# Kernel optimization log

Measured on AMD Instinct MI355X. Metric: run time of the kernel, lower is better.

The kernel has to match this reference:

```python
import jax, jax.numpy as jnp
import numpy as np

N = 1024  # hidden_state
L = 16384  # sequence length


def setup_inputs() -> dict:
    key = jax.random.key(0)
    kA, kB, kC, kd, kX = jax.random.split(key, 5)
    # kaiming_normal_ with nonlinearity='linear': std = 1/sqrt(fan_in) = 1/sqrt(N)
    A = jax.random.normal(kA, (N, N), dtype=jnp.float32) / jnp.sqrt(jnp.float32(N))
    # nn.init.normal_(B, std=(1/N)**0.5)
    B = jax.random.normal(kB, (N, 1), dtype=jnp.float32) / jnp.sqrt(jnp.float32(N))
    # nn.init.normal_(C, std=1.0)
    C = jax.random.normal(kC, (1, N), dtype=jnp.float32)
    D = jnp.ones((1,), dtype=jnp.float32)
    # uniform in [log(min_delta), log(max_delta)]
    log_delta = jax.random.uniform(kd, (1,), dtype=jnp.float32,
                                   minval=jnp.log(1e-3), maxval=jnp.log(1e-1))
    X = jax.random.normal(kX, (L,), dtype=jnp.float32)
    return {"X": X, "A": A, "B": B, "C": C, "D": D, "log_delta": log_delta}


def _discretize(A, B, log_delta):
    n = A.shape[0]
    I = jnp.eye(n, dtype=A.dtype)
    d = jnp.exp(log_delta)  # (1,) broadcasts
    A1 = I - d * 0.5 * A
    A2 = I + d * 0.5 * A
    A1_inv = jnp.linalg.inv(A1)
    dA = A1_inv @ A2                 # (N, N) bilinear (Tustin) discretization
    dB = (A1_inv @ (d * B))[:, 0]    # (N,)
    return dA, dB


def reference(X, A, B, C, D, log_delta):
    """S4 RNN-mode forward: linear state-space recurrence + skip connection."""
    dA, dB = _discretize(A, B, log_delta)
    c = C[0]  # (N,)

    def step(h, x):
        # h_k = dA @ h_{k-1} + dB * x_k ; y_k = C @ h_k
        h = dA @ h + dB * x
        return h, c @ h

    h0 = jnp.zeros((A.shape[0],), dtype=A.dtype)  # cache_h_k starts at zeros
    _, ys = jax.lax.scan(step, h0, X)             # ys: (L,)
    return ys + D * X                              # skip = D * X
```

## Files before the change

kernel.cpp:

```cpp
#include <hip/hip_runtime.h>
#include <math.h>

#define N1 1024
#define NN2 (N1*N1)
#define LL 16384

__global__ __launch_bounds__(256) void k_scale(const float* __restrict__ A,
                                               const float* __restrict__ logd,
                                               float* __restrict__ e) {
    int i = blockIdx.x * 256 + threadIdx.x;
    float d = expf(logd[0]);
    e[i] = 0.5f * d * A[i];
}

__global__ __launch_bounds__(256) void k_add(const float* __restrict__ a,
                                             const float* __restrict__ b,
                                             float* __restrict__ o) {
    int i = blockIdx.x * 256 + threadIdx.x;
    o[i] = a[i] + b[i];
}

__device__ __forceinline__ void chain_part(const float* __restrict__ M,
                                           float* __restrict__ V,
                                           float* __restrict__ CP,
                                           int w, int lkc, int mode, int cb,
                                           float* sV, float (*red)[64]) {
    int kc = 1 << lkc;
    int i = cb >> (4 + lkc);
    int ky = (cb >> 4) & (kc - 1);
    int nx = cb & 15;
    int mlen = N1 >> lkc;
    int m0 = ky * mlen, n0 = nx * 64;
    int t = threadIdx.x;
    const float* Vi = V + (size_t)i * N1 + m0;
    if (t * 4 < mlen) *(float4*)&sV[t * 4] = *(const float4*)&Vi[t * 4];
    __syncthreads();
    int wave = t >> 6, lane = t & 63;
    if (mode == 0) {
        for (int rr = 0; rr < 16; ++rr) {
            int n = n0 + wave * 16 + rr;
            const float* Mr = M + (size_t)n * N1 + m0;
            float acc = 0.f;
            for (int m = lane * 4; m < mlen; m += 256) {
                float4 a = *(const float4*)&Mr[m];
                float4 v = *(const float4*)&sV[m];
                acc += a.x * v.x + a.y * v.y + a.z * v.z + a.w * v.w;
            }
#pragma unroll
            for (int off = 32; off > 0; off >>= 1) acc += __shfl_down(acc, off, 64);
            if (lane == 0) {
                if (kc == 1) V[(size_t)(w + i) * N1 + n] = sV[n] + acc;
                else CP[((size_t)i * kc + ky) * N1 + n] = acc;
            }
        }
    } else {
        int n = n0 + lane;
        int msub = mlen >> 2;
        int mb = wave * msub;
        float acc = 0.f;
#pragma unroll 8
        for (int m = 0; m < msub; ++m)
            acc += sV[mb + m] * M[(size_t)(m0 + mb + m) * N1 + n];
        red[wave][lane] = acc;
        __syncthreads();
        if (t < 64) {
            float s = red[0][t] + red[1][t] + red[2][t] + red[3][t];
            if (kc == 1) V[(size_t)(w + i) * N1 + n0 + t] = sV[n0 + t] + s;
            else CP[((size_t)i * kc + ky) * N1 + n0 + t] = s;
        }
    }
}

__global__ __launch_bounds__(256) void k_fused(const float* __restrict__ Ain,
                                               const float* __restrict__ Bin,
                                               float* __restrict__ part,
                                               float* __restrict__ V,
                                               float* __restrict__ CP,
                                               int w, int lkc, int nchain, int mode) {
    __shared__ float As[2][32][68];
    __shared__ float Bs[2][32][68];
    __shared__ float sV[N1];
    __shared__ float red[4][64];
    int b = blockIdx.x;
    if (b < nchain) {
        chain_part(Ain, V, CP, w, lkc, mode, b, sV, red);
        return;
    }
    int g = b - nchain;
    int t = threadIdx.x;
    int z = g >> 8, ty = (g >> 4) & 15, tx = g & 15;
    int m0 = ty * 64, n0 = tx * 64, kz = z * 512;
    int tm = (t & 15) * 4, tn = (t >> 4) * 4;
    int lmA = t >> 2, lkA = (t & 3) * 8;
    int kbB = t >> 3, nbB = (t & 7) * 8;
    const float* Ap = Ain + (size_t)(m0 + lmA) * N1 + kz + lkA;
    const float* Bp = Bin + (size_t)(kz + kbB) * N1 + n0 + nbB;

    float4 pa0 = *(const float4*)(Ap);
    float4 pa1 = *(const float4*)(Ap + 4);
    float4 pb0 = *(const float4*)(Bp);
    float4 pb1 = *(const float4*)(Bp + 4);
    As[0][lkA + 0][lmA] = pa0.x; As[0][lkA + 1][lmA] = pa0.y;
    As[0][lkA + 2][lmA] = pa0.z; As[0][lkA + 3][lmA] = pa0.w;
    As[0][lkA + 4][lmA] = pa1.x; As[0][lkA + 5][lmA] = pa1.y;
    As[0][lkA + 6][lmA] = pa1.z; As[0][lkA + 7][lmA] = pa1.w;
    *(float4*)&Bs[0][kbB][nbB]     = pb0;
    *(float4*)&Bs[0][kbB][nbB + 4] = pb1;
    __syncthreads();

    float acc[4][4];
#pragma unroll
    for (int i = 0; i < 4; ++i)
#pragma unroll
        for (int j = 0; j < 4; ++j) acc[i][j] = 0.f;

    for (int tt = 0; tt < 16; ++tt) {
        int cur = tt & 1;
        float4 na0, na1, nb0, nb1;
        if (tt < 15) {
            int k0 = (tt + 1) * 32;
            na0 = *(const float4*)(Ap + k0);
            na1 = *(const float4*)(Ap + k0 + 4);
            nb0 = *(const float4*)(Bp + (size_t)k0 * N1);
            nb1 = *(const float4*)(Bp + (size_t)k0 * N1 + 4);
        }
#pragma unroll
        for (int k = 0; k < 32; ++k) {
            float4 a = *(float4*)&As[cur][k][tm];
            float4 bb = *(float4*)&Bs[cur][k][tn];
            acc[0][0] += a.x * bb.x; acc[0][1] += a.x * bb.y; acc[0][2] += a.x * bb.z; acc[0][3] += a.x * bb.w;
            acc[1][0] += a.y * bb.x; acc[1][1] += a.y * bb.y; acc[1][2] += a.y * bb.z; acc[1][3] += a.y * bb.w;
            acc[2][0] += a.z * bb.x; acc[2][1] += a.z * bb.y; acc[2][2] += a.z * bb.z; acc[2][3] += a.z * bb.w;
            acc[3][0] += a.w * bb.x; acc[3][1] += a.w * bb.y; acc[3][2] += a.w * bb.z; acc[3][3] += a.w * bb.w;
        }
        if (tt < 15) {
            int nxt = cur ^ 1;
            As[nxt][lkA + 0][lmA] = na0.x; As[nxt][lkA + 1][lmA] = na0.y;
            As[nxt][lkA + 2][lmA] = na0.z; As[nxt][lkA + 3][lmA] = na0.w;
            As[nxt][lkA + 4][lmA] = na1.x; As[nxt][lkA + 5][lmA] = na1.y;
            As[nxt][lkA + 6][lmA] = na1.z; As[nxt][lkA + 7][lmA] = na1.w;
            *(float4*)&Bs[nxt][kbB][nbB]     = nb0;
            *(float4*)&Bs[nxt][kbB][nbB + 4] = nb1;
            __syncthreads();
        }
    }
    float* Po = part + (size_t)z * NN2;
#pragma unroll
    for (int i = 0; i < 4; ++i) {
        float4 o = {acc[i][0], acc[i][1], acc[i][2], acc[i][3]};
        *(float4*)&Po[(size_t)(m0 + tm + i) * N1 + n0 + tn] = o;
    }
}

__global__ __launch_bounds__(256) void k_cpart(const float* __restrict__ M,
                                               float* __restrict__ V,
                                               float* __restrict__ CP,
                                               int w, int lkc, int mode) {
    __shared__ float sV[N1];
    __shared__ float red[4][64];
    chain_part(M, V, CP, w, lkc, mode, blockIdx.x, sV, red);
}

__global__ __launch_bounds__(256) void k_redu(const float* __restrict__ part,
                                              const float* __restrict__ Aadd,
                                              float* __restrict__ C,
                                              float alpha, float beta,
                                              float* __restrict__ V,
                                              const float* __restrict__ CP,
                                              int w, int kc) {
    int b = blockIdx.x, t = threadIdx.x;
    if (b < 1024) {
        int i = (b * 256 + t) * 4;
        float4 p0 = *(const float4*)&part[i];
        float4 p1 = *(const float4*)&part[NN2 + i];
        float4 av = *(const float4*)&Aadd[i];
        float4 o;
        o.x = alpha * (p0.x + p1.x) + beta * av.x;
        o.y = alpha * (p0.y + p1.y) + beta * av.y;
        o.z = alpha * (p0.z + p1.z) + beta * av.z;
        o.w = alpha * (p0.w + p1.w) + beta * av.w;
        *(float4*)&C[i] = o;
    } else {
        int rb = b - 1024;
        int i = rb >> 2;
        int n = (rb & 3) * 256 + t;
        const float* pp = CP + (size_t)i * kc * N1 + n;
        float s = 0.f;
        for (int c = 0; c < kc; ++c) s += pp[(size_t)c * N1];
        V[(size_t)(w + i) * N1 + n] = V[(size_t)i * N1 + n] + s;
    }
}

__global__ __launch_bounds__(256) void k_initR(const float* __restrict__ Bv,
                                               const float* __restrict__ Cv,
                                               const float* __restrict__ logd,
                                               const float* __restrict__ part,
                                               float* __restrict__ Q,
                                               float* __restrict__ P) {
    int n = blockIdx.x * 256 + threadIdx.x;
    float s = 0.f;
    for (int c = 0; c < 16; ++c) s += part[(size_t)c * N1 + n];
    float d = expf(logd[0]);
    Q[n] = d * (Bv[n] + 0.5f * s);
    P[n] = Cv[n];
}

__global__ __launch_bounds__(256) void k_kdot(const float* __restrict__ P,
                                              const float* __restrict__ Q,
                                              float* __restrict__ K) {
    int t = threadIdx.x;
    int wid = blockIdx.x * 4 + (t >> 6), lane = t & 63;
    int a = wid >> 7, b = wid & 127;
    const float* Pr = P + (size_t)a * N1;
    const float* Qr = Q + (size_t)b * N1;
    float acc = 0.f;
#pragma unroll
    for (int jj = 0; jj < 4; ++jj) {
        int m = jj * 256 + lane * 4;
        float4 p = *(const float4*)&Pr[m];
        float4 q = *(const float4*)&Qr[m];
        acc += p.x * q.x + p.y * q.y + p.z * q.z + p.w * q.w;
    }
#pragma unroll
    for (int off = 32; off > 0; off >>= 1) acc += __shfl_down(acc, off, 64);
    if (lane == 0) K[wid] = acc;
}

__global__ __launch_bounds__(256) void k_conv1(const float* __restrict__ X,
                                               const float* __restrict__ K,
                                               float* __restrict__ part) {
    __shared__ __align__(16) float ks[1280];
    __shared__ __align__(16) float xs[256];
    int bx = blockIdx.x, tt = threadIdx.x;
    int o = 0;
    while (bx >= 2 * (o + 1) * (o + 1) + 2 * (o + 1)) ++o;
    int jt = bx - (2 * o * o + 2 * o);
    int T0 = o * 1024, J0 = jt * 256;
    int mb = T0 - J0 - 255;
    for (int ii = tt; ii < 1280; ii += 256) {
        int m = mb + ii;
        ks[ii] = (m >= 0 && m < LL) ? K[m] : 0.f;
    }
    xs[tt] = X[J0 + tt];
    __syncthreads();

    float acc0 = 0.f, acc1 = 0.f, acc2 = 0.f, acc3 = 0.f;
    int base0 = 4 * tt + 252;
#pragma unroll 4
    for (int jj = 0; jj < 256; jj += 4) {
        float4 xv  = *(const float4*)&xs[jj];
        float4 kv0 = *(const float4*)&ks[base0 - jj];
        float4 kv1 = *(const float4*)&ks[base0 - jj + 4];
        float kk0 = kv0.x, kk1 = kv0.y, kk2 = kv0.z, kk3 = kv0.w;
        float kk4 = kv1.x, kk5 = kv1.y, kk6 = kv1.z;
        acc0 += kk3 * xv.x + kk2 * xv.y + kk1 * xv.z + kk0 * xv.w;
        acc1 += kk4 * xv.x + kk3 * xv.y + kk2 * xv.z + kk1 * xv.w;
        acc2 += kk5 * xv.x + kk4 * xv.y + kk3 * xv.z + kk2 * xv.w;
        acc3 += kk6 * xv.x + kk5 * xv.y + kk4 * xv.z + kk3 * xv.w;
    }
    float4 out = {acc0, acc1, acc2, acc3};
    *(float4*)&part[((size_t)(o * 64 + jt)) * 1024 + 4 * tt] = out;
}

__global__ __launch_bounds__(256) void k_conv2(const float* __restrict__ X,
                                               const float* __restrict__ part,
                                               const float* __restrict__ Dp,
                                               float* __restrict__ Y) {
    int o = blockIdx.x, tt = threadIdx.x;
    int c = 4 * tt;
    float s0 = 0.f, s1 = 0.f, s2 = 0.f, s3 = 0.f;
    int cnt = 4 * o + 4;
    for (int jt = 0; jt < cnt; ++jt) {
        float4 p = *(const float4*)&part[((size_t)(o * 64 + jt)) * 1024 + c];
        s0 += p.x; s1 += p.y; s2 += p.z; s3 += p.w;
    }
    float dsk = Dp[0];
    int t = o * 1024 + c;
    float4 xv = *(const float4*)&X[t];
    float4 out;
    out.x = dsk * xv.x + s0;
    out.y = dsk * xv.y + s1;
    out.z = dsk * xv.z + s2;
    out.w = dsk * xv.w + s3;
    *(float4*)&Y[t] = out;
}

extern "C" void kernel_launch(void* const* d_in, const int* in_sizes, int n_in,
                              void* d_out, int out_size, void* d_ws, size_t ws_size,
                              hipStream_t stream) {
    const float* X    = (const float*)d_in[0];
    const float* A    = (const float*)d_in[1];
    const float* Bv   = (const float*)d_in[2];
    const float* Cv   = (const float*)d_in[3];
    const float* Dp   = (const float*)d_in[4];
    const float* logd = (const float*)d_in[5];
    float* ws = (float*)d_ws;

    float* S0 = ws;
    float* S1 = ws + (size_t)NN2;
    float* S2 = ws + 2*(size_t)NN2;
    float* S3 = ws + 3*(size_t)NN2;
    float* S4 = ws + 4*(size_t)NN2;
    float* MP = ws + 5*(size_t)NN2;
    float* CP = ws + 7*(size_t)NN2;
    float* Q  = CP + 64*(size_t)N1;
    float* P  = Q + 128*(size_t)N1;
    float* Kc = P + 128*(size_t)N1;
    float* Y  = (float*)d_out;

    k_scale<<<4096, 256, 0, stream>>>(A, logd, S0);
    k_fused<<<512, 256, 0, stream>>>(S0, S0, MP, nullptr, nullptr, 0, 0, 0, 0);
    k_redu<<<1024, 256, 0, stream>>>(MP, S0, S1, 1.f, 0.f, nullptr, nullptr, 0, 0);
    k_fused<<<512, 256, 0, stream>>>(S1, S1, MP, nullptr, nullptr, 0, 0, 0, 0);
    k_redu<<<1024, 256, 0, stream>>>(MP, S1, S2, 1.f, 1.f, nullptr, nullptr, 0, 0);
    k_add<<<4096, 256, 0, stream>>>(S0, S1, S3);
    k_fused<<<512, 256, 0, stream>>>(S3, S2, MP, nullptr, nullptr, 0, 0, 0, 0);
    k_redu<<<1024, 256, 0, stream>>>(MP, S3, S4, 2.f, 2.f, nullptr, nullptr, 0, 0);

    k_cpart<<<256, 256, 0, stream>>>(S4, (float*)Bv, CP, 1, 4, 0);
    k_initR<<<4, 256, 0, stream>>>(Bv, Cv, logd, CP, Q, P);

    float* cur = S4;
    float* nxt = S0;
    for (int k = 0; k < 7; ++k) {
        int w = 1 << k;
        int lkc = (w < 16) ? (4 - k) : 0;
        int kc = 1 << lkc;
        int nchain = 16 * kc * w;
        int nR = (kc > 1) ? 4 * w : 0;
        k_fused<<<nchain + 512, 256, 0, stream>>>(cur, cur, MP, Q, CP, w, lkc, nchain, 0);
        k_redu<<<1024 + nR, 256, 0, stream>>>(MP, cur, nxt, 1.f, 2.f, Q, CP, w, kc);
        float* tsw = cur; cur = nxt; nxt = tsw;
    }
    for (int k = 0; k < 6; ++k) {
        int w = 1 << k;
        int lkc = (w < 16) ? (4 - k) : 0;
        int kc = 1 << lkc;
        int nchain = 16 * kc * w;
        int nR = (kc > 1) ? 4 * w : 0;
        k_fused<<<nchain + 512, 256, 0, stream>>>(cur, cur, MP, P, CP, w, lkc, nchain, 1);
        k_redu<<<1024 + nR, 256, 0, stream>>>(MP, cur, nxt, 1.f, 2.f, P, CP, w, kc);
        float* tsw = cur; cur = nxt; nxt = tsw;
    }
    k_cpart<<<1024, 256, 0, stream>>>(cur, P, CP, 64, 0, 1);

    k_kdot<<<4096, 256, 0, stream>>>(P, Q, Kc);
    k_conv1<<<544, 256, 0, stream>>>(X, Kc, MP);
    k_conv2<<<16, 256, 0, stream>>>(X, MP, Dp, Y);
}
```

Before: 795.7 us.

## Replace FP32 SIMT matrix squaring with split-bf16 MFMA GEMMs

Each 1024x1024 matrix product is now computed on bf16 MFMA units. Operands are split into three bf16 pieces and six cross-term MFMAs are issued, approximating FP32 accuracy. The reduction kernel also emits the row-major split and a transposed split of its output, so the next squaring reads pre-packed operands. This removes the FP32 FMA-bound inner loop, at the cost of extra split and transpose writes, more bytes per operand, and a possible precision loss from dropping the small cross terms.

```diff
diff --git a/kernel.cpp b/kernel.cpp
--- a/kernel.cpp
+++ b/kernel.cpp
@@ -4,20 +4,23 @@
 #define N1 1024
 #define NN2 (N1*N1)
 #define LL 16384
-
-__global__ __launch_bounds__(256) void k_scale(const float* __restrict__ A,
-                                               const float* __restrict__ logd,
-                                               float* __restrict__ e) {
-    int i = blockIdx.x * 256 + threadIdx.x;
-    float d = expf(logd[0]);
-    e[i] = 0.5f * d * A[i];
-}
-
-__global__ __launch_bounds__(256) void k_add(const float* __restrict__ a,
-                                             const float* __restrict__ b,
-                                             float* __restrict__ o) {
-    int i = blockIdx.x * 256 + threadIdx.x;
-    o[i] = a[i] + b[i];
+#define PSTR 40
+
+typedef unsigned short u16;
+typedef __attribute__((ext_vector_type(8))) short bffrag;
+typedef __attribute__((ext_vector_type(4))) float f32x4;
+
+__device__ __forceinline__ u16 bf16rne(float x, float& rem) {
+    unsigned u = __float_as_uint(x);
+    u16 h = (u16)((u + 0x7FFF + ((u >> 16) & 1)) >> 16);
+    rem = x - __uint_as_float((unsigned)h << 16);
+    return h;
+}
+__device__ __forceinline__ void split3(float x, u16& h0, u16& h1, u16& h2) {
+    float r1, r2, r3;
+    h0 = bf16rne(x, r1);
+    h1 = bf16rne(r1, r2);
+    h2 = bf16rne(r2, r3);
 }
 
 __device__ __forceinline__ void chain_part(const float* __restrict__ M,
@@ -71,85 +74,98 @@
     }
 }
 
-__global__ __launch_bounds__(256) void k_fused(const float* __restrict__ Ain,
-                                               const float* __restrict__ Bin,
-                                               float* __restrict__ part,
-                                               float* __restrict__ V,
-                                               float* __restrict__ CP,
-                                               int w, int lkc, int nchain, int mode) {
-    __shared__ float As[2][32][68];
-    __shared__ float Bs[2][32][68];
+__global__ __launch_bounds__(256, 1) void k_mfma(const u16* __restrict__ RA,
+                                                 const u16* __restrict__ TB,
+                                                 float* __restrict__ part,
+                                                 const float* __restrict__ Dm,
+                                                 float* __restrict__ V,
+                                                 float* __restrict__ CP,
+                                                 int w, int lkc, int nchain, int mode) {
+    __shared__ u16 Asl[3][64][PSTR];
+    __shared__ u16 Bsl[3][64][PSTR];
     __shared__ float sV[N1];
     __shared__ float red[4][64];
     int b = blockIdx.x;
     if (b < nchain) {
-        chain_part(Ain, V, CP, w, lkc, mode, b, sV, red);
+        chain_part(Dm, V, CP, w, lkc, mode, b, sV, red);
         return;
     }
     int g = b - nchain;
     int t = threadIdx.x;
-    int z = g >> 8, ty = (g >> 4) & 15, tx = g & 15;
+    int z = g >> 8;
+    int ty = (g >> 4) & 15, tx = g & 15;
     int m0 = ty * 64, n0 = tx * 64, kz = z * 512;
-    int tm = (t & 15) * 4, tn = (t >> 4) * 4;
-    int lmA = t >> 2, lkA = (t & 3) * 8;
-    int kbB = t >> 3, nbB = (t & 7) * 8;
-    const float* Ap = Ain + (size_t)(m0 + lmA) * N1 + kz + lkA;
-    const float* Bp = Bin + (size_t)(kz + kbB) * N1 + n0 + nbB;
-
-    float4 pa0 = *(const float4*)(Ap);
-    float4 pa1 = *(const float4*)(Ap + 4);
-    float4 pb0 = *(const float4*)(Bp);
-    float4 pb1 = *(const float4*)(Bp + 4);
-    As[0][lkA + 0][lmA] = pa0.x; As[0][lkA + 1][lmA] = pa0.y;
-    As[0][lkA + 2][lmA] = pa0.z; As[0][lkA + 3][lmA] = pa0.w;
-    As[0][lkA + 4][lmA] = pa1.x; As[0][lkA + 5][lmA] = pa1.y;
-    As[0][lkA + 6][lmA] = pa1.z; As[0][lkA + 7][lmA] = pa1.w;
-    *(float4*)&Bs[0][kbB][nbB]     = pb0;
-    *(float4*)&Bs[0][kbB][nbB + 4] = pb1;
-    __syncthreads();
-
-    float acc[4][4];
-#pragma unroll
-    for (int i = 0; i < 4; ++i)
-#pragma unroll
-        for (int j = 0; j < 4; ++j) acc[i][j] = 0.f;
-
-    for (int tt = 0; tt < 16; ++tt) {
-        int cur = tt & 1;
-        float4 na0, na1, nb0, nb1;
-        if (tt < 15) {
-            int k0 = (tt + 1) * 32;
-            na0 = *(const float4*)(Ap + k0);
-            na1 = *(const float4*)(Ap + k0 + 4);
-            nb0 = *(const float4*)(Bp + (size_t)k0 * N1);
-            nb1 = *(const float4*)(Bp + (size_t)k0 * N1 + 4);
+    int srow = t >> 2, sk = (t & 3) * 8;
+    int wave = t >> 6, lane = t & 63;
+    int mq = (wave & 1) * 32, nq = (wave >> 1) * 32;
+    int fl = lane & 15, kg8 = (lane >> 4) * 8;
+
+    const size_t abase = (size_t)(m0 + srow) * N1 + kz + sk;
+    const size_t bbase = (size_t)(n0 + srow) * N1 + kz + sk;
+
+    uint4 pa[3], pb[3];
+#pragma unroll
+    for (int p = 0; p < 3; ++p) {
+        pa[p] = *(const uint4*)&RA[(size_t)p * NN2 + abase];
+        pb[p] = *(const uint4*)&TB[(size_t)p * NN2 + bbase];
+    }
+
+    f32x4 acc[2][2];
+#pragma unroll
+    for (int mi = 0; mi < 2; ++mi)
+#pragma unroll
+        for (int nj = 0; nj < 2; ++nj) acc[mi][nj] = (f32x4){0.f, 0.f, 0.f, 0.f};
+
+    for (int kt = 0; kt < 16; ++kt) {
+#pragma unroll
+        for (int p = 0; p < 3; ++p) {
+            *(uint4*)&Asl[p][srow][sk] = pa[p];
+            *(uint4*)&Bsl[p][srow][sk] = pb[p];
         }
-#pragma unroll
-        for (int k = 0; k < 32; ++k) {
-            float4 a = *(float4*)&As[cur][k][tm];
-            float4 bb = *(float4*)&Bs[cur][k][tn];
-            acc[0][0] += a.x * bb.x; acc[0][1] += a.x * bb.y; acc[0][2] += a.x * bb.z; acc[0][3] += a.x * bb.w;
-            acc[1][0] += a.y * bb.x; acc[1][1] += a.y * bb.y; acc[1][2] += a.y * bb.z; acc[1][3] += a.y * bb.w;
-            acc[2][0] += a.z * bb.x; acc[2][1] += a.z * bb.y; acc[2][2] += a.z * bb.z; acc[2][3] += a.z * bb.w;
-            acc[3][0] += a.w * bb.x; acc[3][1] += a.w * bb.y; acc[3][2] += a.w * bb.z; acc[3][3] += a.w * bb.w;
+        __syncthreads();
+        if (kt < 15) {
+            size_t koff = (size_t)(kt + 1) * 32;
+#pragma unroll
+            for (int p = 0; p < 3; ++p) {
+                pa[p] = *(const uint4*)&RA[(size_t)p * NN2 + abase + koff];
+                pb[p] = *(const uint4*)&TB[(size_t)p * NN2 + bbase + koff];
+            }
         }
-        if (tt < 15) {
-            int nxt = cur ^ 1;
-            As[nxt][lkA + 0][lmA] = na0.x; As[nxt][lkA + 1][lmA] = na0.y;
-            As[nxt][lkA + 2][lmA] = na0.z; As[nxt][lkA + 3][lmA] = na0.w;
-            As[nxt][lkA + 4][lmA] = na1.x; As[nxt][lkA + 5][lmA] = na1.y;
-            As[nxt][lkA + 6][lmA] = na1.z; As[nxt][lkA + 7][lmA] = na1.w;
-            *(float4*)&Bs[nxt][kbB][nbB]     = nb0;
-            *(float4*)&Bs[nxt][kbB][nbB + 4] = nb1;
-            __syncthreads();
+        bffrag a[2][3], bb[2][3];
+#pragma unroll
+        for (int mi = 0; mi < 2; ++mi)
+#pragma unroll
+            for (int p = 0; p < 3; ++p)
+                a[mi][p] = *(bffrag*)&Asl[p][mq + mi * 16 + fl][kg8];
+#pragma unroll
+        for (int nj = 0; nj < 2; ++nj)
+#pragma unroll
+            for (int q = 0; q < 3; ++q)
+                bb[nj][q] = *(bffrag*)&Bsl[q][nq + nj * 16 + fl][kg8];
+#pragma unroll
+        for (int mi = 0; mi < 2; ++mi)
+#pragma unroll
+            for (int nj = 0; nj < 2; ++nj) {
+                acc[mi][nj] = __builtin_amdgcn_mfma_f32_16x16x32_bf16(a[mi][0], bb[nj][0], acc[mi][nj], 0, 0, 0);
+                acc[mi][nj] = __builtin_amdgcn_mfma_f32_16x16x32_bf16(a[mi][0], bb[nj][1], acc[mi][nj], 0, 0, 0);
+                acc[mi][nj] = __builtin_amdgcn_mfma_f32_16x16x32_bf16(a[mi][1], bb[nj][0], acc[mi][nj], 0, 0, 0);
+                acc[mi][nj] = __builtin_amdgcn_mfma_f32_16x16x32_bf16(a[mi][0], bb[nj][2], acc[mi][nj], 0, 0, 0);
+                acc[mi][nj] = __builtin_amdgcn_mfma_f32_16x16x32_bf16(a[mi][1], bb[nj][1], acc[mi][nj], 0, 0, 0);
+                acc[mi][nj] = __builtin_amdgcn_mfma_f32_16x16x32_bf16(a[mi][2], bb[nj][0], acc[mi][nj], 0, 0, 0);
+            }
+        __syncthreads();
+    }
+    float* Po = part + (size_t)z * NN2;
+#pragma unroll
+    for (int mi = 0; mi < 2; ++mi)
+#pragma unroll
+        for (int nj = 0; nj < 2; ++nj) {
+            int row0 = m0 + mq + mi * 16 + (lane >> 4) * 4;
+            int col = n0 + nq + nj * 16 + fl;
+#pragma unroll
+            for (int r = 0; r < 4; ++r)
+                Po[(size_t)(row0 + r) * N1 + col] = acc[mi][nj][r];
         }
-    }
-    float* Po = part + (size_t)z * NN2;
-#pragma unroll
-    for (int i = 0; i < 4; ++i) {
-        float4 o = {acc[i][0], acc[i][1], acc[i][2], acc[i][3]};
-        *(float4*)&Po[(size_t)(m0 + tm + i) * N1 + n0 + tn] = o;
-    }
 }
 
 __global__ __launch_bounds__(256) void k_cpart(const float* __restrict__ M,
@@ -161,25 +177,103 @@
     chain_part(M, V, CP, w, lkc, mode, blockIdx.x, sV, red);
 }
 
-__global__ __launch_bounds__(256) void k_redu(const float* __restrict__ part,
-                                              const float* __restrict__ Aadd,
-                                              float* __restrict__ C,
-                                              float alpha, float beta,
-                                              float* __restrict__ V,
-                                              const float* __restrict__ CP,
-                                              int w, int kc) {
+__global__ __launch_bounds__(256) void k_split(const float* __restrict__ in1,
+                                               const float* __restrict__ in2,
+                                               const float* __restrict__ logd,
+                                               float c1,
+                                               float* __restrict__ outX,
+                                               u16* __restrict__ Rp,
+                                               u16* __restrict__ Tp) {
+    __shared__ float tile[32][33];
+    int b = blockIdx.x, t = threadIdx.x;
+    int bx = b & 31, by = b >> 5;
+    int x0 = bx * 32, y0 = by * 32;
+    int r = t >> 3, c4 = (t & 7) * 4;
+    float a = c1 * (logd ? expf(logd[0]) : 1.f);
+    size_t idx = (size_t)(y0 + r) * N1 + x0 + c4;
+    float4 v1 = *(const float4*)&in1[idx];
+    float4 X;
+    X.x = a * v1.x; X.y = a * v1.y; X.z = a * v1.z; X.w = a * v1.w;
+    if (in2) {
+        float4 v2 = *(const float4*)&in2[idx];
+        X.x += v2.x; X.y += v2.y; X.z += v2.z; X.w += v2.w;
+    }
+    *(float4*)&outX[idx] = X;
+    ushort4 h0, h1, h2;
+    split3(X.x, h0.x, h1.x, h2.x);
+    split3(X.y, h0.y, h1.y, h2.y);
+    split3(X.z, h0.z, h1.z, h2.z);
+    split3(X.w, h0.w, h1.w, h2.w);
+    *(ushort4*)&Rp[idx] = h0;
+    *(ushort4*)&Rp[(size_t)NN2 + idx] = h1;
+    *(ushort4*)&Rp[2 * (size_t)NN2 + idx] = h2;
+    tile[r][c4 + 0] = X.x; tile[r][c4 + 1] = X.y;
+    tile[r][c4 + 2] = X.z; tile[r][c4 + 3] = X.w;
+    __syncthreads();
+    if (Tp) {
+        int n = t >> 3, mb = (t & 7) * 4;
+        ushort4 g0, g1, g2;
+        float xv0 = tile[mb + 0][n], xv1 = tile[mb + 1][n];
+        float xv2 = tile[mb + 2][n], xv3 = tile[mb + 3][n];
+        split3(xv0, g0.x, g1.x, g2.x);
+        split3(xv1, g0.y, g1.y, g2.y);
+        split3(xv2, g0.z, g1.z, g2.z);
+        split3(xv3, g0.w, g1.w, g2.w);
+        size_t tidx = (size_t)(x0 + n) * N1 + y0 + mb;
+        *(ushort4*)&Tp[tidx] = g0;
+        *(ushort4*)&Tp[(size_t)NN2 + tidx] = g1;
+        *(ushort4*)&Tp[2 * (size_t)NN2 + tidx] = g2;
+    }
+}
+
+__global__ __launch_bounds__(256) void k_redusplit(const float* __restrict__ part,
+                                                   const float* __restrict__ Aadd,
+                                                   float* __restrict__ C,
+                                                   float alpha, float beta,
+                                                   u16* __restrict__ Rp,
+                                                   u16* __restrict__ Tp,
+                                                   float* __restrict__ V,
+                                                   const float* __restrict__ CP,
+                                                   int w, int kc) {
+    __shared__ float tile[32][33];
     int b = blockIdx.x, t = threadIdx.x;
     if (b < 1024) {
-        int i = (b * 256 + t) * 4;
-        float4 p0 = *(const float4*)&part[i];
-        float4 p1 = *(const float4*)&part[NN2 + i];
-        float4 av = *(const float4*)&Aadd[i];
-        float4 o;
-        o.x = alpha * (p0.x + p1.x) + beta * av.x;
-        o.y = alpha * (p0.y + p1.y) + beta * av.y;
-        o.z = alpha * (p0.z + p1.z) + beta * av.z;
-        o.w = alpha * (p0.w + p1.w) + beta * av.w;
-        *(float4*)&C[i] = o;
+        int bx = b & 31, by = b >> 5;
+        int x0 = bx * 32, y0 = by * 32;
+        int r = t >> 3, c4 = (t & 7) * 4;
+        size_t idx = (size_t)(y0 + r) * N1 + x0 + c4;
+        float4 p0 = *(const float4*)&part[idx];
+        float4 p1 = *(const float4*)&part[(size_t)NN2 + idx];
+        float4 av = *(const float4*)&Aadd[idx];
+        float4 X;
+        X.x = alpha * (p0.x + p1.x) + beta * av.x;
+        X.y = alpha * (p0.y + p1.y) + beta * av.y;
+        X.z = alpha * (p0.z + p1.z) + beta * av.z;
+        X.w = alpha * (p0.w + p1.w) + beta * av.w;
+        *(float4*)&C[idx] = X;
+        ushort4 h0, h1, h2;
+        split3(X.x, h0.x, h1.x, h2.x);
+        split3(X.y, h0.y, h1.y, h2.y);
+        split3(X.z, h0.z, h1.z, h2.z);
+        split3(X.w, h0.w, h1.w, h2.w);
+        *(ushort4*)&Rp[idx] = h0;
+        *(ushort4*)&Rp[(size_t)NN2 + idx] = h1;
+        *(ushort4*)&Rp[2 * (size_t)NN2 + idx] = h2;
+        tile[r][c4 + 0] = X.x; tile[r][c4 + 1] = X.y;
+        tile[r][c4 + 2] = X.z; tile[r][c4 + 3] = X.w;
+        __syncthreads();
+        int n = t >> 3, mb = (t & 7) * 4;
+        ushort4 g0, g1, g2;
+        float xv0 = tile[mb + 0][n], xv1 = tile[mb + 1][n];
+        float xv2 = tile[mb + 2][n], xv3 = tile[mb + 3][n];
+        split3(xv0, g0.x, g1.x, g2.x);
+        split3(xv1, g0.y, g1.y, g2.y);
+        split3(xv2, g0.z, g1.z, g2.z);
+        split3(xv3, g0.w, g1.w, g2.w);
+        size_t tidx = (size_t)(x0 + n) * N1 + y0 + mb;
+        *(ushort4*)&Tp[tidx] = g0;
+        *(ushort4*)&Tp[(size_t)NN2 + tidx] = g1;
+        *(ushort4*)&Tp[2 * (size_t)NN2 + tidx] = g2;
     } else {
         int rb = b - 1024;
         int i = rb >> 2;
@@ -302,23 +396,26 @@
     float* S3 = ws + 3*(size_t)NN2;
     float* S4 = ws + 4*(size_t)NN2;
     float* MP = ws + 5*(size_t)NN2;
-    float* CP = ws + 7*(size_t)NN2;
-    float* Q  = CP + 64*(size_t)N1;
-    float* P  = Q + 128*(size_t)N1;
-    float* Kc = P + 128*(size_t)N1;
+    float* CPb = ws + 7*(size_t)NN2;
+    float* Qv = CPb + 64*(size_t)N1;
+    float* Pv = Qv + 128*(size_t)N1;
+    float* Kc = Pv + 128*(size_t)N1;
+    u16*   R0 = (u16*)(Kc + LL);
+    u16*   R1 = R0 + 3*(size_t)NN2;
+    u16*   T0 = R1 + 3*(size_t)NN2;
     float* Y  = (float*)d_out;
 
-    k_scale<<<4096, 256, 0, stream>>>(A, logd, S0);
-    k_fused<<<512, 256, 0, stream>>>(S0, S0, MP, nullptr, nullptr, 0, 0, 0, 0);
-    k_redu<<<1024, 256, 0, stream>>>(MP, S0, S1, 1.f, 0.f, nullptr, nullptr, 0, 0);
-    k_fused<<<512, 256, 0, stream>>>(S1, S1, MP, nullptr, nullptr, 0, 0, 0, 0);
-    k_redu<<<1024, 256, 0, stream>>>(MP, S1, S2, 1.f, 1.f, nullptr, nullptr, 0, 0);
-    k_add<<<4096, 256, 0, stream>>>(S0, S1, S3);
-    k_fused<<<512, 256, 0, stream>>>(S3, S2, MP, nullptr, nullptr, 0, 0, 0, 0);
-    k_redu<<<1024, 256, 0, stream>>>(MP, S3, S4, 2.f, 2.f, nullptr, nullptr, 0, 0);
-
-    k_cpart<<<256, 256, 0, stream>>>(S4, (float*)Bv, CP, 1, 4, 0);
-    k_initR<<<4, 256, 0, stream>>>(Bv, Cv, logd, CP, Q, P);
+    k_split<<<1024, 256, 0, stream>>>(A, nullptr, logd, 0.5f, S0, R0, T0);
+    k_mfma<<<512, 256, 0, stream>>>(R0, T0, MP, nullptr, nullptr, nullptr, 0, 0, 0, 0);
+    k_redusplit<<<1024, 256, 0, stream>>>(MP, S0, S1, 1.f, 0.f, R0, T0, nullptr, nullptr, 0, 1);
+    k_mfma<<<512, 256, 0, stream>>>(R0, T0, MP, nullptr, nullptr, nullptr, 0, 0, 0, 0);
+    k_redusplit<<<1024, 256, 0, stream>>>(MP, S1, S2, 1.f, 1.f, R0, T0, nullptr, nullptr, 0, 1);
+    k_split<<<1024, 256, 0, stream>>>(S1, S0, nullptr, 1.f, S3, R1, nullptr);
+    k_mfma<<<512, 256, 0, stream>>>(R1, T0, MP, nullptr, nullptr, nullptr, 0, 0, 0, 0);
+    k_redusplit<<<1024, 256, 0, stream>>>(MP, S3, S4, 2.f, 2.f, R0, T0, nullptr, nullptr, 0, 1);
+
+    k_cpart<<<256, 256, 0, stream>>>(S4, (float*)Bv, CPb, 1, 4, 0);
+    k_initR<<<4, 256, 0, stream>>>(Bv, Cv, logd, CPb, Qv, Pv);
 
     float* cur = S4;
     float* nxt = S0;
@@ -328,8 +425,8 @@
         int kc = 1 << lkc;
         int nchain = 16 * kc * w;
         int nR = (kc > 1) ? 4 * w : 0;
-        k_fused<<<nchain + 512, 256, 0, stream>>>(cur, cur, MP, Q, CP, w, lkc, nchain, 0);
-        k_redu<<<1024 + nR, 256, 0, stream>>>(MP, cur, nxt, 1.f, 2.f, Q, CP, w, kc);
+        k_mfma<<<nchain + 512, 256, 0, stream>>>(R0, T0, MP, cur, Qv, CPb, w, lkc, nchain, 0);
+        k_redusplit<<<1024 + nR, 256, 0, stream>>>(MP, cur, nxt, 1.f, 2.f, R0, T0, Qv, CPb, w, kc);
         float* tsw = cur; cur = nxt; nxt = tsw;
     }
     for (int k = 0; k < 6; ++k) {
@@ -338,13 +435,13 @@
         int kc = 1 << lkc;
         int nchain = 16 * kc * w;
         int nR = (kc > 1) ? 4 * w : 0;
-        k_fused<<<nchain + 512, 256, 0, stream>>>(cur, cur, MP, P, CP, w, lkc, nchain, 1);
-        k_redu<<<1024 + nR, 256, 0, stream>>>(MP, cur, nxt, 1.f, 2.f, P, CP, w, kc);
+        k_mfma<<<nchain + 512, 256, 0, stream>>>(R0, T0, MP, cur, Pv, CPb, w, lkc, nchain, 1);
+        k_redusplit<<<1024 + nR, 256, 0, stream>>>(MP, cur, nxt, 1.f, 2.f, R0, T0, Pv, CPb, w, kc);
         float* tsw = cur; cur = nxt; nxt = tsw;
     }
-    k_cpart<<<1024, 256, 0, stream>>>(cur, P, CP, 64, 0, 1);
-
-    k_kdot<<<4096, 256, 0, stream>>>(P, Q, Kc);
+    k_cpart<<<1024, 256, 0, stream>>>(cur, Pv, CPb, 64, 0, 1);
+
+    k_kdot<<<4096, 256, 0, stream>>>(Pv, Qv, Kc);
     k_conv1<<<544, 256, 0, stream>>>(X, Kc, MP);
     k_conv2<<<16, 256, 0, stream>>>(X, MP, Dp, Y);
 }
```

Measured after the change: 1.280 ms. 60.9% more time.

## Fuse split-K reduction into GEMM via atomic tile flags and trim power chain

Applied to the files above, without the earlier changes.

Each split-K GEMM block now increments a per-tile atomic counter after writing its partial. The second block to finish sums both partials and applies the alpha/beta epilogue in place, which removes the separate reduction kernel after every squaring step. The chain-vector updates are simplified to a single full-length pass per block, and the transposed-chain squaring stops after four steps. The last three doublings are replaced by repeated matrix-vector applications with the final power. The change relies on threadfence/atomic ordering across blocks and on resetting the flags correctly, and it adds more small kernel launches at the tail.

```diff
diff --git a/kernel.cpp b/kernel.cpp
--- a/kernel.cpp
+++ b/kernel.cpp
@@ -5,12 +5,18 @@
 #define NN2 (N1*N1)
 #define LL 16384
 
-__global__ __launch_bounds__(256) void k_scale(const float* __restrict__ A,
-                                               const float* __restrict__ logd,
-                                               float* __restrict__ e) {
-    int i = blockIdx.x * 256 + threadIdx.x;
-    float d = expf(logd[0]);
-    e[i] = 0.5f * d * A[i];
+__global__ __launch_bounds__(256) void k_prep(const float* __restrict__ A,
+                                              const float* __restrict__ logd,
+                                              float* __restrict__ e,
+                                              int* __restrict__ flags) {
+    int b = blockIdx.x, t = threadIdx.x;
+    if (b < 4096) {
+        int i = b * 256 + t;
+        float d = expf(logd[0]);
+        e[i] = 0.5f * d * A[i];
+    } else {
+        if (t < 256) flags[t] = 0;
+    }
 }
 
 __global__ __launch_bounds__(256) void k_add(const float* __restrict__ a,
@@ -20,92 +26,85 @@
     o[i] = a[i] + b[i];
 }
 
-__device__ __forceinline__ void chain_part(const float* __restrict__ M,
-                                           float* __restrict__ V,
-                                           float* __restrict__ CP,
-                                           int w, int lkc, int mode, int cb,
-                                           float* sV, float (*red)[64]) {
-    int kc = 1 << lkc;
-    int i = cb >> (4 + lkc);
-    int ky = (cb >> 4) & (kc - 1);
-    int nx = cb & 15;
-    int mlen = N1 >> lkc;
-    int m0 = ky * mlen, n0 = nx * 64;
-    int t = threadIdx.x;
-    const float* Vi = V + (size_t)i * N1 + m0;
-    if (t * 4 < mlen) *(float4*)&sV[t * 4] = *(const float4*)&Vi[t * 4];
-    __syncthreads();
-    int wave = t >> 6, lane = t & 63;
-    if (mode == 0) {
-        for (int rr = 0; rr < 16; ++rr) {
-            int n = n0 + wave * 16 + rr;
-            const float* Mr = M + (size_t)n * N1 + m0;
+__global__ __launch_bounds__(256) void k_fused(const float* __restrict__ GA,
+                                               const float* __restrict__ GB,
+                                               float* __restrict__ MP,
+                                               float* __restrict__ Cout,
+                                               const float* __restrict__ Aadd,
+                                               float alpha, float beta,
+                                               int* __restrict__ flags,
+                                               const float* __restrict__ Dm,
+                                               float* __restrict__ V,
+                                               int w, int mode) {
+    __shared__ __align__(16) char smem[34816];
+    __shared__ int sflag;
+    int b = blockIdx.x, t = threadIdx.x;
+
+    if (b >= 512) {
+        int cb = b - 512;
+        int i = cb >> 4, nx = cb & 15, n0 = nx * 64;
+        float* sV  = (float*)smem;
+        float* red = (float*)(smem + 4096);
+        const float* Vi = V + (size_t)i * N1;
+        *(float4*)&sV[t * 4] = *(const float4*)&Vi[t * 4];
+        __syncthreads();
+        int wave = t >> 6, lane = t & 63;
+        if (mode == 0) {
+            for (int rr = 0; rr < 16; ++rr) {
+                int n = n0 + wave * 16 + rr;
+                const float* Mr = Dm + (size_t)n * N1;
+                float acc = 0.f;
+#pragma unroll
+                for (int jj = 0; jj < 4; ++jj) {
+                    int m = jj * 256 + lane * 4;
+                    float4 a = *(const float4*)&Mr[m];
+                    float4 v = *(const float4*)&sV[m];
+                    acc += a.x * v.x + a.y * v.y + a.z * v.z + a.w * v.w;
+                }
+#pragma unroll
+                for (int off = 32; off > 0; off >>= 1) acc += __shfl_down(acc, off, 64);
+                if (lane == 0) V[(size_t)(w + i) * N1 + n] = sV[n] + acc;
+            }
+        } else {
+            int n = n0 + lane;
+            int mb = wave * 256;
             float acc = 0.f;
-            for (int m = lane * 4; m < mlen; m += 256) {
-                float4 a = *(const float4*)&Mr[m];
-                float4 v = *(const float4*)&sV[m];
-                acc += a.x * v.x + a.y * v.y + a.z * v.z + a.w * v.w;
+#pragma unroll 8
+            for (int m = 0; m < 256; ++m)
+                acc += sV[mb + m] * Dm[(size_t)(mb + m) * N1 + n];
+            red[wave * 64 + lane] = acc;
+            __syncthreads();
+            if (t < 64) {
+                float s = red[t] + red[64 + t] + red[128 + t] + red[192 + t];
+                V[(size_t)(w + i) * N1 + n0 + t] = sV[n0 + t] + s;
             }
-#pragma unroll
-            for (int off = 32; off > 0; off >>= 1) acc += __shfl_down(acc, off, 64);
-            if (lane == 0) {
-                if (kc == 1) V[(size_t)(w + i) * N1 + n] = sV[n] + acc;
-                else CP[((size_t)i * kc + ky) * N1 + n] = acc;
-            }
-        }
-    } else {
-        int n = n0 + lane;
-        int msub = mlen >> 2;
-        int mb = wave * msub;
-        float acc = 0.f;
-#pragma unroll 8
-        for (int m = 0; m < msub; ++m)
-            acc += sV[mb + m] * M[(size_t)(m0 + mb + m) * N1 + n];
-        red[wave][lane] = acc;
-        __syncthreads();
-        if (t < 64) {
-            float s = red[0][t] + red[1][t] + red[2][t] + red[3][t];
-            if (kc == 1) V[(size_t)(w + i) * N1 + n0 + t] = sV[n0 + t] + s;
-            else CP[((size_t)i * kc + ky) * N1 + n0 + t] = s;
-        }
-    }
-}
-
-__global__ __launch_bounds__(256) void k_fused(const float* __restrict__ Ain,
-                                               const float* __restrict__ Bin,
-                                               float* __restrict__ part,
-                                               float* __restrict__ V,
-                                               float* __restrict__ CP,
-                                               int w, int lkc, int nchain, int mode) {
-    __shared__ float As[2][32][68];
-    __shared__ float Bs[2][32][68];
-    __shared__ float sV[N1];
-    __shared__ float red[4][64];
-    int b = blockIdx.x;
-    if (b < nchain) {
-        chain_part(Ain, V, CP, w, lkc, mode, b, sV, red);
+        }
         return;
     }
-    int g = b - nchain;
-    int t = threadIdx.x;
+
+    float* As = (float*)smem;
+    float* Bs = (float*)(smem + 17408);
+#define AS(bf, k, m) As[((bf) * 32 + (k)) * 68 + (m)]
+#define BS(bf, k, m) Bs[((bf) * 32 + (k)) * 68 + (m)]
+    int g = b;
     int z = g >> 8, ty = (g >> 4) & 15, tx = g & 15;
     int m0 = ty * 64, n0 = tx * 64, kz = z * 512;
     int tm = (t & 15) * 4, tn = (t >> 4) * 4;
     int lmA = t >> 2, lkA = (t & 3) * 8;
     int kbB = t >> 3, nbB = (t & 7) * 8;
-    const float* Ap = Ain + (size_t)(m0 + lmA) * N1 + kz + lkA;
-    const float* Bp = Bin + (size_t)(kz + kbB) * N1 + n0 + nbB;
+    const float* Ap = GA + (size_t)(m0 + lmA) * N1 + kz + lkA;
+    const float* Bp = GB + (size_t)(kz + kbB) * N1 + n0 + nbB;
 
     float4 pa0 = *(const float4*)(Ap);
     float4 pa1 = *(const float4*)(Ap + 4);
     float4 pb0 = *(const float4*)(Bp);
     float4 pb1 = *(const float4*)(Bp + 4);
-    As[0][lkA + 0][lmA] = pa0.x; As[0][lkA + 1][lmA] = pa0.y;
-    As[0][lkA + 2][lmA] = pa0.z; As[0][lkA + 3][lmA] = pa0.w;
-    As[0][lkA + 4][lmA] = pa1.x; As[0][lkA + 5][lmA] = pa1.y;
-    As[0][lkA + 6][lmA] = pa1.z; As[0][lkA + 7][lmA] = pa1.w;
-    *(float4*)&Bs[0][kbB][nbB]     = pb0;
-    *(float4*)&Bs[0][kbB][nbB + 4] = pb1;
+    AS(0, lkA + 0, lmA) = pa0.x; AS(0, lkA + 1, lmA) = pa0.y;
+    AS(0, lkA + 2, lmA) = pa0.z; AS(0, lkA + 3, lmA) = pa0.w;
+    AS(0, lkA + 4, lmA) = pa1.x; AS(0, lkA + 5, lmA) = pa1.y;
+    AS(0, lkA + 6, lmA) = pa1.z; AS(0, lkA + 7, lmA) = pa1.w;
+    *(float4*)&BS(0, kbB, nbB)     = pb0;
+    *(float4*)&BS(0, kbB, nbB + 4) = pb1;
     __syncthreads();
 
     float acc[4][4];
@@ -126,80 +125,117 @@
         }
 #pragma unroll
         for (int k = 0; k < 32; ++k) {
-            float4 a = *(float4*)&As[cur][k][tm];
-            float4 bb = *(float4*)&Bs[cur][k][tn];
+            float4 a = *(float4*)&AS(cur, k, tm);
+            float4 bb = *(float4*)&BS(cur, k, tn);
             acc[0][0] += a.x * bb.x; acc[0][1] += a.x * bb.y; acc[0][2] += a.x * bb.z; acc[0][3] += a.x * bb.w;
             acc[1][0] += a.y * bb.x; acc[1][1] += a.y * bb.y; acc[1][2] += a.y * bb.z; acc[1][3] += a.y * bb.w;
             acc[2][0] += a.z * bb.x; acc[2][1] += a.z * bb.y; acc[2][2] += a.z * bb.z; acc[2][3] += a.z * bb.w;
             acc[3][0] += a.w * bb.x; acc[3][1] += a.w * bb.y; acc[3][2] += a.w * bb.z; acc[3][3] += a.w * bb.w;
         }
         if (tt < 15) {
-            int nxt = cur ^ 1;
-            As[nxt][lkA + 0][lmA] = na0.x; As[nxt][lkA + 1][lmA] = na0.y;
-            As[nxt][lkA + 2][lmA] = na0.z; As[nxt][lkA + 3][lmA] = na0.w;
-            As[nxt][lkA + 4][lmA] = na1.x; As[nxt][lkA + 5][lmA] = na1.y;
-            As[nxt][lkA + 6][lmA] = na1.z; As[nxt][lkA + 7][lmA] = na1.w;
-            *(float4*)&Bs[nxt][kbB][nbB]     = nb0;
-            *(float4*)&Bs[nxt][kbB][nbB + 4] = nb1;
+            int nx_ = cur ^ 1;
+            AS(nx_, lkA + 0, lmA) = na0.x; AS(nx_, lkA + 1, lmA) = na0.y;
+            AS(nx_, lkA + 2, lmA) = na0.z; AS(nx_, lkA + 3, lmA) = na0.w;
+            AS(nx_, lkA + 4, lmA) = na1.x; AS(nx_, lkA + 5, lmA) = na1.y;
+            AS(nx_, lkA + 6, lmA) = na1.z; AS(nx_, lkA + 7, lmA) = na1.w;
+            *(float4*)&BS(nx_, kbB, nbB)     = nb0;
+            *(float4*)&BS(nx_, kbB, nbB + 4) = nb1;
             __syncthreads();
         }
     }
-    float* Po = part + (size_t)z * NN2;
+    float* Po = MP + (size_t)z * NN2;
 #pragma unroll
     for (int i = 0; i < 4; ++i) {
         float4 o = {acc[i][0], acc[i][1], acc[i][2], acc[i][3]};
         *(float4*)&Po[(size_t)(m0 + tm + i) * N1 + n0 + tn] = o;
     }
-}
-
-__global__ __launch_bounds__(256) void k_cpart(const float* __restrict__ M,
-                                               float* __restrict__ V,
-                                               float* __restrict__ CP,
-                                               int w, int lkc, int mode) {
+    __threadfence();
+    if (t == 0) sflag = atomicAdd(&flags[ty * 16 + tx], 1);
+    __syncthreads();
+    if (sflag == 1) {
+        __threadfence();
+        const float* Pq = MP + (size_t)(1 - z) * NN2;
+#pragma unroll
+        for (int i = 0; i < 4; ++i) {
+            size_t ri = (size_t)(m0 + tm + i) * N1 + n0 + tn;
+            float4 oth = *(const float4*)&Pq[ri];
+            float4 mine = {acc[i][0], acc[i][1], acc[i][2], acc[i][3]};
+            float4 p0 = (z == 0) ? mine : oth;
+            float4 p1 = (z == 0) ? oth : mine;
+            float4 av = *(const float4*)&Aadd[ri];
+            float4 o;
+            o.x = alpha * (p0.x + p1.x) + beta * av.x;
+            o.y = alpha * (p0.y + p1.y) + beta * av.y;
+            o.z = alpha * (p0.z + p1.z) + beta * av.z;
+            o.w = alpha * (p0.w + p1.w) + beta * av.w;
+            *(float4*)&Cout[ri] = o;
+        }
+        if (t == 0) flags[ty * 16 + tx] = 0;
+    }
+#undef AS
+#undef BS
+}
+
+__global__ __launch_bounds__(256) void k_capply(const float* __restrict__ M,
+                                                const float* __restrict__ src,
+                                                float* __restrict__ dst) {
     __shared__ float sV[N1];
     __shared__ float red[4][64];
-    chain_part(M, V, CP, w, lkc, mode, blockIdx.x, sV, red);
-}
-
-__global__ __launch_bounds__(256) void k_redu(const float* __restrict__ part,
-                                              const float* __restrict__ Aadd,
-                                              float* __restrict__ C,
-                                              float alpha, float beta,
-                                              float* __restrict__ V,
-                                              const float* __restrict__ CP,
-                                              int w, int kc) {
     int b = blockIdx.x, t = threadIdx.x;
-    if (b < 1024) {
-        int i = (b * 256 + t) * 4;
-        float4 p0 = *(const float4*)&part[i];
-        float4 p1 = *(const float4*)&part[NN2 + i];
-        float4 av = *(const float4*)&Aadd[i];
-        float4 o;
-        o.x = alpha * (p0.x + p1.x) + beta * av.x;
-        o.y = alpha * (p0.y + p1.y) + beta * av.y;
-        o.z = alpha * (p0.z + p1.z) + beta * av.z;
-        o.w = alpha * (p0.w + p1.w) + beta * av.w;
-        *(float4*)&C[i] = o;
-    } else {
-        int rb = b - 1024;
-        int i = rb >> 2;
-        int n = (rb & 3) * 256 + t;
-        const float* pp = CP + (size_t)i * kc * N1 + n;
-        float s = 0.f;
-        for (int c = 0; c < kc; ++c) s += pp[(size_t)c * N1];
-        V[(size_t)(w + i) * N1 + n] = V[(size_t)i * N1 + n] + s;
+    int i = b >> 4, nx = b & 15, n0 = nx * 64;
+    const float* Si = src + (size_t)i * N1;
+    *(float4*)&sV[t * 4] = *(const float4*)&Si[t * 4];
+    __syncthreads();
+    int wave = t >> 6, lane = t & 63;
+    int n = n0 + lane;
+    int mb = wave * 256;
+    float acc = 0.f;
+#pragma unroll 8
+    for (int m = 0; m < 256; ++m)
+        acc += sV[mb + m] * M[(size_t)(mb + m) * N1 + n];
+    red[wave][lane] = acc;
+    __syncthreads();
+    if (t < 64) {
+        float s = red[0][t] + red[1][t] + red[2][t] + red[3][t];
+        dst[(size_t)i * N1 + n0 + t] = sV[n0 + t] + s;
+    }
+}
+
+__global__ __launch_bounds__(256) void k_cpart(const float* __restrict__ M,
+                                               const float* __restrict__ Bv,
+                                               float* __restrict__ CP) {
+    __shared__ float sV[64];
+    int cb = blockIdx.x, t = threadIdx.x;
+    int ky = (cb >> 4) & 15, nx = cb & 15;
+    int m0 = ky * 64, n0 = nx * 64;
+    if (t < 16) *(float4*)&sV[t * 4] = *(const float4*)&Bv[m0 + t * 4];
+    __syncthreads();
+    int wave = t >> 6, lane = t & 63;
+    for (int rr = 0; rr < 16; ++rr) {
+        int n = n0 + wave * 16 + rr;
+        const float* Mr = M + (size_t)n * N1 + m0;
+        float acc = 0.f;
+        if (lane < 16) {
+            int m = lane * 4;
+            float4 a = *(const float4*)&Mr[m];
+            float4 v = *(const float4*)&sV[m];
+            acc = a.x * v.x + a.y * v.y + a.z * v.z + a.w * v.w;
+        }
+#pragma unroll
+        for (int off = 8; off > 0; off >>= 1) acc += __shfl_down(acc, off, 64);
+        if (lane == 0) CP[(size_t)ky * N1 + n] = acc;
     }
 }
 
 __global__ __launch_bounds__(256) void k_initR(const float* __restrict__ Bv,
                                                const float* __restrict__ Cv,
                                                const float* __restrict__ logd,
-                                               const float* __restrict__ part,
+                                               const float* __restrict__ CP,
                                                float* __restrict__ Q,
                                                float* __restrict__ P) {
     int n = blockIdx.x * 256 + threadIdx.x;
     float s = 0.f;
-    for (int c = 0; c < 16; ++c) s += part[(size_t)c * N1 + n];
+    for (int c = 0; c < 16; ++c) s += CP[(size_t)c * N1 + n];
     float d = expf(logd[0]);
     Q[n] = d * (Bv[n] + 0.5f * s);
     P[n] = Cv[n];
@@ -298,53 +334,49 @@
 
     float* S0 = ws;
     float* S1 = ws + (size_t)NN2;
-    float* S2 = ws + 2*(size_t)NN2;
-    float* S3 = ws + 3*(size_t)NN2;
-    float* S4 = ws + 4*(size_t)NN2;
-    float* MP = ws + 5*(size_t)NN2;
-    float* CP = ws + 7*(size_t)NN2;
-    float* Q  = CP + 64*(size_t)N1;
-    float* P  = Q + 128*(size_t)N1;
-    float* Kc = P + 128*(size_t)N1;
+    float* S2 = ws + 2 * (size_t)NN2;
+    float* S3 = ws + 3 * (size_t)NN2;
+    float* S4 = ws + 4 * (size_t)NN2;
+    float* MP = ws + 5 * (size_t)NN2;
+    float* CP = ws + 7 * (size_t)NN2;
+    float* T1 = CP + 64 * (size_t)N1;
+    float* T2 = T1 + 64 * (size_t)N1;
+    float* Qv = T2 + 64 * (size_t)N1;
+    float* Pv = Qv + 128 * (size_t)N1;
+    float* Kc = Pv + 128 * (size_t)N1;
+    int* flags = (int*)(Kc + LL);
     float* Y  = (float*)d_out;
 
-    k_scale<<<4096, 256, 0, stream>>>(A, logd, S0);
-    k_fused<<<512, 256, 0, stream>>>(S0, S0, MP, nullptr, nullptr, 0, 0, 0, 0);
-    k_redu<<<1024, 256, 0, stream>>>(MP, S0, S1, 1.f, 0.f, nullptr, nullptr, 0, 0);
-    k_fused<<<512, 256, 0, stream>>>(S1, S1, MP, nullptr, nullptr, 0, 0, 0, 0);
-    k_redu<<<1024, 256, 0, stream>>>(MP, S1, S2, 1.f, 1.f, nullptr, nullptr, 0, 0);
+    k_prep<<<4097, 256, 0, stream>>>(A, logd, S0, flags);
+    k_fused<<<512, 256, 0, stream>>>(S0, S0, MP, S1, S0, 1.f, 0.f, flags, S0, nullptr, 0, 0);
+    k_fused<<<512, 256, 0, stream>>>(S1, S1, MP, S2, S1, 1.f, 1.f, flags, S0, nullptr, 0, 0);
     k_add<<<4096, 256, 0, stream>>>(S0, S1, S3);
-    k_fused<<<512, 256, 0, stream>>>(S3, S2, MP, nullptr, nullptr, 0, 0, 0, 0);
-    k_redu<<<1024, 256, 0, stream>>>(MP, S3, S4, 2.f, 2.f, nullptr, nullptr, 0, 0);
-
-    k_cpart<<<256, 256, 0, stream>>>(S4, (float*)Bv, CP, 1, 4, 0);
-    k_initR<<<4, 256, 0, stream>>>(Bv, Cv, logd, CP, Q, P);
+    k_fused<<<512, 256, 0, stream>>>(S3, S2, MP, S4, S3, 2.f, 2.f, flags, S0, nullptr, 0, 0);
+
+    k_cpart<<<256, 256, 0, stream>>>(S4, Bv, CP);
+    k_initR<<<4, 256, 0, stream>>>(Bv, Cv, logd, CP, Qv, Pv);
 
     float* cur = S4;
     float* nxt = S0;
     for (int k = 0; k < 7; ++k) {
         int w = 1 << k;
-        int lkc = (w < 16) ? (4 - k) : 0;
-        int kc = 1 << lkc;
-        int nchain = 16 * kc * w;
-        int nR = (kc > 1) ? 4 * w : 0;
-        k_fused<<<nchain + 512, 256, 0, stream>>>(cur, cur, MP, Q, CP, w, lkc, nchain, 0);
-        k_redu<<<1024 + nR, 256, 0, stream>>>(MP, cur, nxt, 1.f, 2.f, Q, CP, w, kc);
-        float* tsw = cur; cur = nxt; nxt = tsw;
-    }
-    for (int k = 0; k < 6; ++k) {
+        k_fused<<<512 + 16 * w, 256, 0, stream>>>(cur, cur, MP, nxt, cur, 1.f, 2.f, flags, cur, Qv, w, 0);
+        float* ts = cur; cur = nxt; nxt = ts;
+    }
+    for (int k = 0; k < 4; ++k) {
         int w = 1 << k;
-        int lkc = (w < 16) ? (4 - k) : 0;
-        int kc = 1 << lkc;
-        int nchain = 16 * kc * w;
-        int nR = (kc > 1) ? 4 * w : 0;
-        k_fused<<<nchain + 512, 256, 0, stream>>>(cur, cur, MP, P, CP, w, lkc, nchain, 1);
-        k_redu<<<1024 + nR, 256, 0, stream>>>(MP, cur, nxt, 1.f, 2.f, P, CP, w, kc);
-        float* tsw = cur; cur = nxt; nxt = tsw;
-    }
-    k_cpart<<<1024, 256, 0, stream>>>(cur, P, CP, 64, 0, 1);
-
-    k_kdot<<<4096, 256, 0, stream>>>(P, Q, Kc);
+        k_fused<<<512 + 16 * w, 256, 0, stream>>>(cur, cur, MP, nxt, cur, 1.f, 2.f, flags, cur, Pv, w, 1);
+        float* ts = cur; cur = nxt; nxt = ts;
+    }
+    k_capply<<<256, 256, 0, stream>>>(cur, Pv, Pv + 16 * (size_t)N1);
+    k_capply<<<512, 256, 0, stream>>>(cur, Pv, T1);
+    k_capply<<<512, 256, 0, stream>>>(cur, T1, Pv + 32 * (size_t)N1);
+    k_capply<<<1024, 256, 0, stream>>>(cur, Pv, T1);
+    k_capply<<<1024, 256, 0, stream>>>(cur, T1, T2);
+    k_capply<<<1024, 256, 0, stream>>>(cur, T2, T1);
+    k_capply<<<1024, 256, 0, stream>>>(cur, T1, Pv + 64 * (size_t)N1);
+
+    k_kdot<<<4096, 256, 0, stream>>>(Pv, Qv, Kc);
     k_conv1<<<544, 256, 0, stream>>>(X, Kc, MP);
     k_conv2<<<16, 256, 0, stream>>>(X, MP, Dp, Y);
 }
```

Result: slower. 1.996 ms (+150.8%).
